# Kernel tuning notes

Measured on AMD Instinct MI355X. Metric: run time of the kernel, lower is better.

## Reference

```python
import jax, jax.numpy as jnp
import numpy as np

V = 1_000_000
NODE_DIM = 128
HIDDEN = 128
OUT_DIM = 128
GLOBAL_DIM = 64
N_GRAPH = 50_000


def setup_inputs() -> dict:
    key = jax.random.key(0)
    ks = jax.random.split(key, 10)
    s1 = 1.0 / np.sqrt(NODE_DIM)
    s3 = 1.0 / np.sqrt(2 * HIDDEN + GLOBAL_DIM)
    return {
        "x": jax.random.normal(ks[0], (V, NODE_DIM), dtype=jnp.float32),
        "node2graph": jax.random.randint(ks[1], (V,), 0, N_GRAPH, dtype=jnp.int64),
        "global_x": jax.random.normal(ks[2], (N_GRAPH, GLOBAL_DIM), dtype=jnp.float32),
        "W1": jax.random.uniform(ks[3], (HIDDEN, NODE_DIM), jnp.float32, -s1, s1),
        "b1": jax.random.uniform(ks[4], (HIDDEN,), jnp.float32, -s1, s1),
        "W2": jax.random.uniform(ks[5], (HIDDEN, NODE_DIM), jnp.float32, -s1, s1),
        "b2": jax.random.uniform(ks[6], (HIDDEN,), jnp.float32, -s1, s1),
        "W3": jax.random.uniform(ks[7], (OUT_DIM, 2 * HIDDEN + GLOBAL_DIM), jnp.float32, -s3, s3),
        "b3": jax.random.uniform(ks[8], (OUT_DIM,), jnp.float32, -s3, s3),
    }


def reference(x, node2graph, global_x, W1, b1, W2, b2, W3, b3):
    # gated projection: linear1(x) * sigmoid(linear2(x))   [V, H]
    h = (x @ W1.T + b1) * jax.nn.sigmoid(x @ W2.T + b2)
    # segment sum / mean over graphs   [N, H]
    Z1 = jax.ops.segment_sum(h, node2graph, num_segments=N_GRAPH)
    counts = jax.ops.segment_sum(jnp.ones((h.shape[0],), h.dtype), node2graph,
                                 num_segments=N_GRAPH)
    Z2 = Z1 / jnp.maximum(counts, 1.0)[:, None]
    Z = jnp.concatenate([Z1, Z2, global_x], axis=-1)  # [N, 2H+Fg]
    return jax.nn.relu(Z @ W3.T + b3)  # [N, OUT_DIM]
```

## Files before the change

kernel.cpp:

```cpp
#include <hip/hip_runtime.h>
#include <cmath>

#define V_NODES  1000000
#define NODE_DIM 128
#define HIDDEN   128
#define OUT_DIM  128
#define GDIM     64
#define NGRAPH   50000

typedef unsigned short u16;
typedef __attribute__((ext_vector_type(8))) short          short8;
typedef __attribute__((ext_vector_type(8))) unsigned short ushort8;
typedef __attribute__((ext_vector_type(8))) __bf16         bf16x8;
typedef __attribute__((ext_vector_type(4))) float          f32x4;

__device__ __forceinline__ u16 f2bf(float f) {
  unsigned u = __builtin_bit_cast(unsigned, f);
  u += 0x7fff + ((u >> 16) & 1);
  return (u16)(u >> 16);
}

__device__ __forceinline__ f32x4 mfma_bf16(bf16x8 a, bf16x8 b, f32x4 c) {
  return __builtin_amdgcn_mfma_f32_16x16x32_bf16(a, b, c, 0, 0, 0);
}

__global__ __launch_bounds__(256) void convert_weights(
    const float* __restrict__ W1, const float* __restrict__ W2,
    const float* __restrict__ W3,
    u16* __restrict__ w1b, u16* __restrict__ w2b, u16* __restrict__ w3b) {
  int i = blockIdx.x * 256 + threadIdx.x;
  if (i < NODE_DIM * HIDDEN) {
    w1b[i] = f2bf(W1[i]);
    w2b[i] = f2bf(W2[i]);
  }
  if (i < OUT_DIM * (2 * HIDDEN + GDIM)) w3b[i] = f2bf(W3[i]);
}

__global__ __launch_bounds__(256) void count_k(
    const int* __restrict__ n2g, int* __restrict__ cnt) {
  int i = blockIdx.x * 256 + threadIdx.x;
  if (i < V_NODES) atomicAdd(&cnt[n2g[i]], 1);
}

__global__ __launch_bounds__(1024) void scan_k(
    const int* __restrict__ cnt, int* __restrict__ head) {
  __shared__ int ls[1024];
  const int t = threadIdx.x;
  const int base = t * 49;
  int s = 0;
#pragma unroll 7
  for (int j = 0; j < 49; ++j) {
    int idx = base + j;
    if (idx < NGRAPH) s += cnt[idx];
  }
  ls[t] = s;
  __syncthreads();
  for (int d = 1; d < 1024; d <<= 1) {
    int v = (t >= d) ? ls[t - d] : 0;
    __syncthreads();
    ls[t] += v;
    __syncthreads();
  }
  int run = ls[t] - s;
#pragma unroll 7
  for (int j = 0; j < 49; ++j) {
    int idx = base + j;
    if (idx < NGRAPH) {
      head[idx] = run;
      run += cnt[idx];
    }
  }
}

__global__ __launch_bounds__(256) void scatter_k(
    const int* __restrict__ n2g, int* __restrict__ head,
    int* __restrict__ ord, u16* __restrict__ gs) {
  int i = blockIdx.x * 256 + threadIdx.x;
  if (i < V_NODES) {
    int g = n2g[i];
    int pos = atomicAdd(&head[g], 1);
    ord[pos] = i;
    gs[pos] = (u16)g;
  }
}

__global__ __launch_bounds__(256, 2) void gather_gated(
    const float* __restrict__ x, const int* __restrict__ ord,
    const u16* __restrict__ gs,
    const u16* __restrict__ w1b, const u16* __restrict__ w2b,
    const float* __restrict__ b1, const float* __restrict__ b2,
    float* __restrict__ Z1) {
  extern __shared__ u16 lds[];
  u16* sW1 = lds;
  u16* sW2 = lds + 16384;
  const int tid = threadIdx.x;

#pragma unroll
  for (int i = 0; i < 8; ++i) {
    int m = i * 256 + tid;
    int n = m >> 4, c = m & 15;
    int p = c ^ (n & 15);
    *(ushort8*)(sW1 + n * 128 + p * 8) = *(const ushort8*)(w1b + m * 8);
    *(ushort8*)(sW2 + n * 128 + p * 8) = *(const ushort8*)(w2b + m * 8);
  }
  __syncthreads();

  const int lane = tid & 63;
  const int wv   = tid >> 6;
  const int q    = lane >> 4;
  const int mr   = lane & 15;
  const int rowbase = blockIdx.x * 64 + wv * 16;
  const int node    = ord[rowbase + mr];

  f32x4 acc1[8] = {};
  f32x4 acc2[8] = {};

#pragma unroll
  for (int kc = 0; kc < 4; ++kc) {
    const int k0 = kc * 32;
    const float* ap = x + (size_t)node * NODE_DIM + k0 + q * 8;
    float4 a0 = *(const float4*)ap;
    float4 a1 = *(const float4*)(ap + 4);
    bf16x8 af;
    af[0] = (__bf16)a0.x; af[1] = (__bf16)a0.y; af[2] = (__bf16)a0.z; af[3] = (__bf16)a0.w;
    af[4] = (__bf16)a1.x; af[5] = (__bf16)a1.y; af[6] = (__bf16)a1.z; af[7] = (__bf16)a1.w;

    const int p = ((k0 >> 3) + q) ^ mr;
#pragma unroll
    for (int t = 0; t < 8; ++t) {
      const int n = t * 16 + mr;
      short8 bs1 = *(const short8*)(sW1 + n * 128 + p * 8);
      short8 bs2 = *(const short8*)(sW2 + n * 128 + p * 8);
      acc1[t] = mfma_bf16(af, __builtin_bit_cast(bf16x8, bs1), acc1[t]);
      acc2[t] = mfma_bf16(af, __builtin_bit_cast(bf16x8, bs2), acc2[t]);
    }
  }

  const int rb4 = rowbase + q * 4;
  const int gq0 = gs[rb4 + 0];
  const int gq1 = gs[rb4 + 1];
  const int gq2 = gs[rb4 + 2];
  const int gq3 = gs[rb4 + 3];
  const int gprev = (q > 0) ? (int)gs[rb4 - 1] : -1;
  const int gnext = (q < 3) ? (int)gs[rb4 + 4] : -1;

  const int uni_own  = (gq0 == gq1) & (gq1 == gq2) & (gq2 == gq3);
  const int conn_own = (gq0 == gprev) ? 1 : 0;
  const int conn_p   = __shfl_up(conn_own, 16, 64);
  const int uni_p    = __shfl_up(uni_own, 16, 64);
  const int conn_p2  = __shfl_up(conn_own, 32, 64);
  const int uni_p2   = __shfl_up(uni_own, 32, 64);
  const bool c1 = conn_own != 0;
  const bool c2 = c1 && (uni_p  && conn_p);
  const bool c3 = c2 && (uni_p2 && conn_p2);

#pragma unroll
  for (int t = 0; t < 8; ++t) {
    const int col = t * 16 + mr;
    const float bb1 = b1[col];
    const float bb2 = b2[col];

    float l1, l2;
    l1 = acc1[t][0] + bb1; l2 = acc2[t][0] + bb2; const float h0 = l1 / (1.0f + __expf(-l2));
    l1 = acc1[t][1] + bb1; l2 = acc2[t][1] + bb2; const float h1 = l1 / (1.0f + __expf(-l2));
    l1 = acc1[t][2] + bb1; l2 = acc2[t][2] + bb2; const float h2 = l1 / (1.0f + __expf(-l2));
    l1 = acc1[t][3] + bb1; l2 = acc2[t][3] + bb2; const float h3 = l1 / (1.0f + __expf(-l2));

    float ts = h3;
    if (gq2 == gq3) { ts += h2; if (gq1 == gq3) { ts += h1; if (gq0 == gq3) ts += h0; } }
    const float ts1 = __shfl_up(ts, 16, 64);
    const float ts2 = __shfl_up(ts, 32, 64);
    const float ts3 = __shfl_up(ts, 48, 64);
    float carry = 0.0f;
    if (c1) { carry = ts1; if (c2) { carry += ts2; if (c3) carry += ts3; } }

    float run = carry + h0;
    if (gq1 != gq0) { atomicAdd(Z1 + (size_t)gq0 * HIDDEN + col, run); run = h1; } else run += h1;
    if (gq2 != gq1) { atomicAdd(Z1 + (size_t)gq1 * HIDDEN + col, run); run = h2; } else run += h2;
    if (gq3 != gq2) { atomicAdd(Z1 + (size_t)gq2 * HIDDEN + col, run); run = h3; } else run += h3;
    if (gnext != gq3) atomicAdd(Z1 + (size_t)gq3 * HIDDEN + col, run);
  }
}

__global__ __launch_bounds__(256, 4) void readout_k(
    const float* __restrict__ Z1, const int* __restrict__ cnt,
    const float* __restrict__ gx, const u16* __restrict__ w3b,
    const float* __restrict__ b3, float* __restrict__ out) {
  const int tid  = threadIdx.x;
  const int lane = tid & 63;
  const int wv   = tid >> 6;
  const int q    = lane >> 4;
  const int mr   = lane & 15;
  const int rowbase = blockIdx.x * 64 + wv * 16;
  const int arow    = rowbase + mr;
  const bool rowok  = arow < NGRAPH;

  float inv = 0.0f;
  if (rowok) inv = 1.0f / fmaxf((float)cnt[arow], 1.0f);

  f32x4 acc[8] = {};

#pragma unroll
  for (int kc = 0; kc < 10; ++kc) {
    const int k0 = kc * 32;
    float av[8];
    if (rowok) {
      if (k0 < 128) {
        const float* p = Z1 + (size_t)arow * HIDDEN + k0 + q * 8;
        float4 a0 = *(const float4*)p;
        float4 a1 = *(const float4*)(p + 4);
        av[0]=a0.x; av[1]=a0.y; av[2]=a0.z; av[3]=a0.w;
        av[4]=a1.x; av[5]=a1.y; av[6]=a1.z; av[7]=a1.w;
      } else if (k0 < 256) {
        const float* p = Z1 + (size_t)arow * HIDDEN + (k0 - 128) + q * 8;
        float4 a0 = *(const float4*)p;
        float4 a1 = *(const float4*)(p + 4);
        av[0]=a0.x*inv; av[1]=a0.y*inv; av[2]=a0.z*inv; av[3]=a0.w*inv;
        av[4]=a1.x*inv; av[5]=a1.y*inv; av[6]=a1.z*inv; av[7]=a1.w*inv;
      } else {
        const float* p = gx + (size_t)arow * GDIM + (k0 - 256) + q * 8;
        float4 a0 = *(const float4*)p;
        float4 a1 = *(const float4*)(p + 4);
        av[0]=a0.x; av[1]=a0.y; av[2]=a0.z; av[3]=a0.w;
        av[4]=a1.x; av[5]=a1.y; av[6]=a1.z; av[7]=a1.w;
      }
    } else {
#pragma unroll
      for (int j = 0; j < 8; ++j) av[j] = 0.0f;
    }
    bf16x8 af;
#pragma unroll
    for (int j = 0; j < 8; ++j) af[j] = (__bf16)av[j];

#pragma unroll
    for (int t = 0; t < 8; ++t) {
      const int n = t * 16 + mr;
      short8 bs = *(const short8*)(w3b + (size_t)n * (2 * HIDDEN + GDIM) + k0 + q * 8);
      acc[t] = mfma_bf16(af, __builtin_bit_cast(bf16x8, bs), acc[t]);
    }
  }

#pragma unroll
  for (int t = 0; t < 8; ++t) {
    const int col = t * 16 + mr;
    const float bb = b3[col];
#pragma unroll
    for (int r = 0; r < 4; ++r) {
      const int row = rowbase + q * 4 + r;
      if (row < NGRAPH)
        out[(size_t)row * OUT_DIM + col] = fmaxf(acc[t][r] + bb, 0.0f);
    }
  }
}

extern "C" void kernel_launch(void* const* d_in, const int* in_sizes, int n_in,
                              void* d_out, int out_size, void* d_ws, size_t ws_size,
                              hipStream_t stream) {
  const float* x   = (const float*)d_in[0];
  const int*   n2g = (const int*)d_in[1];
  const float* gx  = (const float*)d_in[2];
  const float* W1  = (const float*)d_in[3];
  const float* b1  = (const float*)d_in[4];
  const float* W2  = (const float*)d_in[5];
  const float* b2  = (const float*)d_in[6];
  const float* W3  = (const float*)d_in[7];
  const float* b3  = (const float*)d_in[8];
  float* out = (float*)d_out;

  char* ws = (char*)d_ws;
  u16*   w1b  = (u16*)(ws);
  u16*   w2b  = (u16*)(ws + 32768);
  u16*   w3b  = (u16*)(ws + 65536);
  float* Z1   = (float*)(ws + 147456);
  int*   cnt  = (int*)(ws + 147456 + (size_t)NGRAPH * HIDDEN * 4);
  int*   head = (int*)(ws + 147456 + (size_t)NGRAPH * HIDDEN * 4 + (size_t)NGRAPH * 4);
  int*   ord  = (int*)(ws + 147456 + (size_t)NGRAPH * HIDDEN * 4 + (size_t)NGRAPH * 8);
  u16*   gs   = (u16*)(ws + 147456 + (size_t)NGRAPH * HIDDEN * 4 + (size_t)NGRAPH * 8
                          + (size_t)V_NODES * 4);

  hipMemsetAsync(ws + 147456, 0,
                 (size_t)NGRAPH * HIDDEN * 4 + (size_t)NGRAPH * 4, stream);

  convert_weights<<<160, 256, 0, stream>>>(W1, W2, W3, w1b, w2b, w3b);

  const int nb = (V_NODES + 255) / 256;
  count_k<<<nb, 256, 0, stream>>>(n2g, cnt);
  scan_k<<<1, 1024, 0, stream>>>(cnt, head);
  scatter_k<<<nb, 256, 0, stream>>>(n2g, head, ord, gs);

  gather_gated<<<V_NODES / 64, 256, 2 * 16384 * sizeof(u16), stream>>>(
      x, ord, gs, w1b, w2b, b1, b2, Z1);

  readout_k<<<(NGRAPH + 63) / 64, 256, 0, stream>>>(Z1, cnt, gx, w3b, b3, out);
}
```

Measured before the change: 1.180 ms.

## Pre-swizzle weights, double gather block size, overlap x loads with LDS staging

Weights are stored in their swizzled LDS layout when they are converted, so the gather kernel can copy them into LDS linearly. Gather blocks grow to 512 threads and 128 rows, which halves the number of per-block weight copies. The x rows are now loaded before the barrier so those loads overlap with LDS staging. Count and scatter use int4 loads, and the separate sorted graph-id array is dropped in favour of reading n2g[node] and shuffling it across lanes. The costs are a random 4-byte read per row, guards for the partial last block, and possible occupancy pressure from holding the x fragments in registers across the barrier.

Measured after the change: 1.014 ms. 14.0% less time.

```diff
diff --git a/kernel.cpp b/kernel.cpp
--- a/kernel.cpp
+++ b/kernel.cpp
@@ -27,11 +27,15 @@
 __global__ __launch_bounds__(256) void convert_weights(
     const float* __restrict__ W1, const float* __restrict__ W2,
     const float* __restrict__ W3,
-    u16* __restrict__ w1b, u16* __restrict__ w2b, u16* __restrict__ w3b) {
+    u16* __restrict__ w1s, u16* __restrict__ w2s, u16* __restrict__ w3b) {
   int i = blockIdx.x * 256 + threadIdx.x;
   if (i < NODE_DIM * HIDDEN) {
-    w1b[i] = f2bf(W1[i]);
-    w2b[i] = f2bf(W2[i]);
+    int d = i >> 3, j = i & 7;
+    int n = d >> 4, p = d & 15;
+    int c = p ^ (n & 15);
+    int src = n * 128 + c * 8 + j;
+    w1s[i] = f2bf(W1[src]);
+    w2s[i] = f2bf(W2[src]);
   }
   if (i < OUT_DIM * (2 * HIDDEN + GDIM)) w3b[i] = f2bf(W3[i]);
 }
@@ -39,7 +43,13 @@
 __global__ __launch_bounds__(256) void count_k(
     const int* __restrict__ n2g, int* __restrict__ cnt) {
   int i = blockIdx.x * 256 + threadIdx.x;
-  if (i < V_NODES) atomicAdd(&cnt[n2g[i]], 1);
+  if (i * 4 < V_NODES) {
+    int4 g = *(const int4*)(n2g + i * 4);
+    atomicAdd(&cnt[g.x], 1);
+    atomicAdd(&cnt[g.y], 1);
+    atomicAdd(&cnt[g.z], 1);
+    atomicAdd(&cnt[g.w], 1);
+  }
 }
 
 __global__ __launch_bounds__(1024) void scan_k(
@@ -74,75 +84,67 @@
 
 __global__ __launch_bounds__(256) void scatter_k(
     const int* __restrict__ n2g, int* __restrict__ head,
-    int* __restrict__ ord, u16* __restrict__ gs) {
+    int* __restrict__ ord) {
   int i = blockIdx.x * 256 + threadIdx.x;
-  if (i < V_NODES) {
-    int g = n2g[i];
-    int pos = atomicAdd(&head[g], 1);
-    ord[pos] = i;
-    gs[pos] = (u16)g;
-  }
-}
-
-__global__ __launch_bounds__(256, 2) void gather_gated(
+  if (i * 4 < V_NODES) {
+    int4 g = *(const int4*)(n2g + i * 4);
+    int base = i * 4;
+    ord[atomicAdd(&head[g.x], 1)] = base;
+    ord[atomicAdd(&head[g.y], 1)] = base + 1;
+    ord[atomicAdd(&head[g.z], 1)] = base + 2;
+    ord[atomicAdd(&head[g.w], 1)] = base + 3;
+  }
+}
+
+__global__ __launch_bounds__(512, 4) void gather_gated(
     const float* __restrict__ x, const int* __restrict__ ord,
-    const u16* __restrict__ gs,
-    const u16* __restrict__ w1b, const u16* __restrict__ w2b,
+    const int* __restrict__ n2g,
+    const u16* __restrict__ w1s, const u16* __restrict__ w2s,
     const float* __restrict__ b1, const float* __restrict__ b2,
     float* __restrict__ Z1) {
   extern __shared__ u16 lds[];
   u16* sW1 = lds;
   u16* sW2 = lds + 16384;
-  const int tid = threadIdx.x;
-
-#pragma unroll
-  for (int i = 0; i < 8; ++i) {
-    int m = i * 256 + tid;
-    int n = m >> 4, c = m & 15;
-    int p = c ^ (n & 15);
-    *(ushort8*)(sW1 + n * 128 + p * 8) = *(const ushort8*)(w1b + m * 8);
-    *(ushort8*)(sW2 + n * 128 + p * 8) = *(const ushort8*)(w2b + m * 8);
-  }
-  __syncthreads();
-
+  const int tid  = threadIdx.x;
   const int lane = tid & 63;
   const int wv   = tid >> 6;
   const int q    = lane >> 4;
   const int mr   = lane & 15;
-  const int rowbase = blockIdx.x * 64 + wv * 16;
-  const int node    = ord[rowbase + mr];
-
-  f32x4 acc1[8] = {};
-  f32x4 acc2[8] = {};
-
+  const int rowbase = blockIdx.x * 128 + wv * 16;
+  const int rowpos  = rowbase + mr;
+  const int rp      = rowpos < V_NODES ? rowpos : V_NODES - 1;
+
+  const int node = ord[rp];
+
+#pragma unroll
+  for (int i = 0; i < 4; ++i) {
+    int m = i * 512 + tid;
+    *(ushort8*)(sW1 + m * 8) = *(const ushort8*)(w1s + m * 8);
+    *(ushort8*)(sW2 + m * 8) = *(const ushort8*)(w2s + m * 8);
+  }
+
+  const int g_own = (rowpos < V_NODES) ? n2g[node] : -1;
+
+  bf16x8 af[4];
 #pragma unroll
   for (int kc = 0; kc < 4; ++kc) {
-    const int k0 = kc * 32;
-    const float* ap = x + (size_t)node * NODE_DIM + k0 + q * 8;
+    const float* ap = x + (size_t)node * NODE_DIM + kc * 32 + q * 8;
     float4 a0 = *(const float4*)ap;
     float4 a1 = *(const float4*)(ap + 4);
-    bf16x8 af;
-    af[0] = (__bf16)a0.x; af[1] = (__bf16)a0.y; af[2] = (__bf16)a0.z; af[3] = (__bf16)a0.w;
-    af[4] = (__bf16)a1.x; af[5] = (__bf16)a1.y; af[6] = (__bf16)a1.z; af[7] = (__bf16)a1.w;
-
-    const int p = ((k0 >> 3) + q) ^ mr;
-#pragma unroll
-    for (int t = 0; t < 8; ++t) {
-      const int n = t * 16 + mr;
-      short8 bs1 = *(const short8*)(sW1 + n * 128 + p * 8);
-      short8 bs2 = *(const short8*)(sW2 + n * 128 + p * 8);
-      acc1[t] = mfma_bf16(af, __builtin_bit_cast(bf16x8, bs1), acc1[t]);
-      acc2[t] = mfma_bf16(af, __builtin_bit_cast(bf16x8, bs2), acc2[t]);
-    }
-  }
-
-  const int rb4 = rowbase + q * 4;
-  const int gq0 = gs[rb4 + 0];
-  const int gq1 = gs[rb4 + 1];
-  const int gq2 = gs[rb4 + 2];
-  const int gq3 = gs[rb4 + 3];
-  const int gprev = (q > 0) ? (int)gs[rb4 - 1] : -1;
-  const int gnext = (q < 3) ? (int)gs[rb4 + 4] : -1;
+    af[kc][0] = (__bf16)a0.x; af[kc][1] = (__bf16)a0.y;
+    af[kc][2] = (__bf16)a0.z; af[kc][3] = (__bf16)a0.w;
+    af[kc][4] = (__bf16)a1.x; af[kc][5] = (__bf16)a1.y;
+    af[kc][6] = (__bf16)a1.z; af[kc][7] = (__bf16)a1.w;
+  }
+
+  const int gq0 = __shfl(g_own, q * 4 + 0, 64);
+  const int gq1 = __shfl(g_own, q * 4 + 1, 64);
+  const int gq2 = __shfl(g_own, q * 4 + 2, 64);
+  const int gq3 = __shfl(g_own, q * 4 + 3, 64);
+  const int gpv = __shfl(g_own, (q * 4 - 1) & 63, 64);
+  const int gnv = __shfl(g_own, (q * 4 + 4) & 15, 64);
+  const int gprev = (q > 0) ? gpv : -1;
+  const int gnext = (q < 3) ? gnv : -1;
 
   const int uni_own  = (gq0 == gq1) & (gq1 == gq2) & (gq2 == gq3);
   const int conn_own = (gq0 == gprev) ? 1 : 0;
@@ -154,6 +156,24 @@
   const bool c2 = c1 && (uni_p  && conn_p);
   const bool c3 = c2 && (uni_p2 && conn_p2);
 
+  __syncthreads();
+
+  f32x4 acc1[8] = {};
+  f32x4 acc2[8] = {};
+
+#pragma unroll
+  for (int kc = 0; kc < 4; ++kc) {
+    const int p = (kc * 4 + q) ^ mr;
+#pragma unroll
+    for (int t = 0; t < 8; ++t) {
+      const int n = t * 16 + mr;
+      short8 bs1 = *(const short8*)(sW1 + n * 128 + p * 8);
+      short8 bs2 = *(const short8*)(sW2 + n * 128 + p * 8);
+      acc1[t] = mfma_bf16(af[kc], __builtin_bit_cast(bf16x8, bs1), acc1[t]);
+      acc2[t] = mfma_bf16(af[kc], __builtin_bit_cast(bf16x8, bs2), acc2[t]);
+    }
+  }
+
 #pragma unroll
   for (int t = 0; t < 8; ++t) {
     const int col = t * 16 + mr;
@@ -175,10 +195,10 @@
     if (c1) { carry = ts1; if (c2) { carry += ts2; if (c3) carry += ts3; } }
 
     float run = carry + h0;
-    if (gq1 != gq0) { atomicAdd(Z1 + (size_t)gq0 * HIDDEN + col, run); run = h1; } else run += h1;
-    if (gq2 != gq1) { atomicAdd(Z1 + (size_t)gq1 * HIDDEN + col, run); run = h2; } else run += h2;
-    if (gq3 != gq2) { atomicAdd(Z1 + (size_t)gq2 * HIDDEN + col, run); run = h3; } else run += h3;
-    if (gnext != gq3) atomicAdd(Z1 + (size_t)gq3 * HIDDEN + col, run);
+    if (gq1 != gq0) { if (gq0 >= 0) atomicAdd(Z1 + (size_t)gq0 * HIDDEN + col, run); run = h1; } else run += h1;
+    if (gq2 != gq1) { if (gq1 >= 0) atomicAdd(Z1 + (size_t)gq1 * HIDDEN + col, run); run = h2; } else run += h2;
+    if (gq3 != gq2) { if (gq2 >= 0) atomicAdd(Z1 + (size_t)gq2 * HIDDEN + col, run); run = h3; } else run += h3;
+    if (gnext != gq3) { if (gq3 >= 0) atomicAdd(Z1 + (size_t)gq3 * HIDDEN + col, run); }
   }
 }
 
@@ -268,28 +288,26 @@
   float* out = (float*)d_out;
 
   char* ws = (char*)d_ws;
-  u16*   w1b  = (u16*)(ws);
-  u16*   w2b  = (u16*)(ws + 32768);
+  u16*   w1s  = (u16*)(ws);
+  u16*   w2s  = (u16*)(ws + 32768);
   u16*   w3b  = (u16*)(ws + 65536);
   float* Z1   = (float*)(ws + 147456);
   int*   cnt  = (int*)(ws + 147456 + (size_t)NGRAPH * HIDDEN * 4);
   int*   head = (int*)(ws + 147456 + (size_t)NGRAPH * HIDDEN * 4 + (size_t)NGRAPH * 4);
   int*   ord  = (int*)(ws + 147456 + (size_t)NGRAPH * HIDDEN * 4 + (size_t)NGRAPH * 8);
-  u16*   gs   = (u16*)(ws + 147456 + (size_t)NGRAPH * HIDDEN * 4 + (size_t)NGRAPH * 8
-                          + (size_t)V_NODES * 4);
 
   hipMemsetAsync(ws + 147456, 0,
                  (size_t)NGRAPH * HIDDEN * 4 + (size_t)NGRAPH * 4, stream);
 
-  convert_weights<<<160, 256, 0, stream>>>(W1, W2, W3, w1b, w2b, w3b);
-
-  const int nb = (V_NODES + 255) / 256;
-  count_k<<<nb, 256, 0, stream>>>(n2g, cnt);
+  convert_weights<<<160, 256, 0, stream>>>(W1, W2, W3, w1s, w2s, w3b);
+
+  const int nb4 = (V_NODES / 4 + 255) / 256;
+  count_k<<<nb4, 256, 0, stream>>>(n2g, cnt);
   scan_k<<<1, 1024, 0, stream>>>(cnt, head);
-  scatter_k<<<nb, 256, 0, stream>>>(n2g, head, ord, gs);
-
-  gather_gated<<<V_NODES / 64, 256, 2 * 16384 * sizeof(u16), stream>>>(
-      x, ord, gs, w1b, w2b, b1, b2, Z1);
+  scatter_k<<<nb4, 256, 0, stream>>>(n2g, head, ord);
+
+  gather_gated<<<(V_NODES + 127) / 128, 512, 2 * 16384 * sizeof(u16), stream>>>(
+      x, ord, n2g, w1s, w2s, b1, b2, Z1);
 
   readout_k<<<(NGRAPH + 63) / 64, 256, 0, stream>>>(Z1, cnt, gx, w3b, b3, out);
 }
```
